# Kernel tuning notes

Measured on AMD Instinct MI355X. Metric: run time of the kernel, lower is better.

Reference implementation:

```python
import jax, jax.numpy as jnp
import numpy as np

B, S, HID, NH, K = 4, 1500, 1024, 16, 64
DH = HID // NH  # 64


def _rel_bias(pos_emb, length):
    # pos_emb: [2K+1, d]; Shaw-style relative position embedding lookup -> [S, S, d]
    kk = (pos_emb.shape[0] - 1) // 2
    idx = jnp.arange(length)
    dist = jnp.clip(idx[None, :] - idx[:, None], -kk, kk) + kk
    return pos_emb[dist]


def setup_inputs() -> dict:
    key = jax.random.key(0)
    ks = jax.random.split(key, 12)
    sq = 1.0 / np.sqrt(HID)
    inp = {
        "query": jax.random.normal(ks[0], (B, S, HID), jnp.float32),
        "key": jax.random.normal(ks[1], (B, S, HID), jnp.float32),
        "value": jax.random.normal(ks[2], (B, S, HID), jnp.float32),
        # per-head QKV projections stacked over heads: [NH, HID, DH]
        "Wq": jax.random.normal(ks[3], (NH, HID, DH), jnp.float32) * sq,
        "bq": jnp.zeros((NH, DH), jnp.float32),
        "Wk": jax.random.normal(ks[4], (NH, HID, DH), jnp.float32) * sq,
        "bk": jnp.zeros((NH, DH), jnp.float32),
        "Wv": jax.random.normal(ks[5], (NH, HID, DH), jnp.float32) * sq,
        "bv": jnp.zeros((NH, DH), jnp.float32),
        # relative position tables [2K+1, DH]
        "pos_k": jax.random.normal(ks[6], (2 * K + 1, DH), jnp.float32) * 0.1,
        "pos_v": jax.random.normal(ks[7], (2 * K + 1, DH), jnp.float32) * 0.1,
        # output projection
        "W_fc": jax.random.normal(ks[8], (HID, HID), jnp.float32) * sq,
        "b_fc": jnp.zeros((HID,), jnp.float32),
    }
    return inp


def reference(query, key, value, Wq, bq, Wk, bk, Wv, bv, pos_k, pos_v, W_fc, b_fc):
    seq = query.shape[1]
    k_bias = _rel_bias(pos_k, seq)  # [S, S, DH]
    v_bias = _rel_bias(pos_v, seq)  # [S, S, DH]

    # batched per-head projections: [B, NH, S, DH]
    q = jnp.einsum('bsh,nhd->bnsd', query, Wq) + bq[None, :, None, :]
    k = jnp.einsum('bsh,nhd->bnsd', key, Wk) + bk[None, :, None, :]
    v = jnp.einsum('bsh,nhd->bnsd', value, Wv) + bv[None, :, None, :]

    attn_1 = jnp.einsum('bnqd,bnkd->bnqk', q, k)
    attn_2 = jnp.einsum('bnqd,qkd->bnqk', q, k_bias)  # Shaw relative key bias
    scores = (attn_1 + attn_2) / jnp.sqrt(jnp.float32(DH))
    w = jax.nn.softmax(scores, axis=-1)  # [B, NH, S, S]

    values_1 = jnp.einsum('bnqk,bnkd->bnqd', w, v)
    values_2 = jnp.einsum('bnqk,qkd->bnqd', w, v_bias)  # Shaw relative value bias
    heads = values_1 + values_2  # [B, NH, S, DH]

    # concat heads in head order -> [B, S, HID]
    hidden = jnp.transpose(heads, (0, 2, 1, 3)).reshape(query.shape[0], seq, -1)
    return hidden @ W_fc + b_fc
```

## Files before the change

kernel.cpp:

```cpp
#include <hip/hip_runtime.h>
#include <stdint.h>

typedef unsigned short u16;
typedef __attribute__((ext_vector_type(8))) short bf16x8;
typedef __attribute__((ext_vector_type(4))) float f32x4;

#define MFMA16(a, b, c) __builtin_amdgcn_mfma_f32_16x16x32_bf16(a, b, c, 0, 0, 0)

__device__ __forceinline__ u16 f2bf(float x) {
  union { float f; uint32_t u; } v; v.f = x;
  uint32_t r = (v.u + 0x7FFFu + ((v.u >> 16) & 1u)) >> 16;
  return (u16)r;
}
__device__ __forceinline__ float bf2f(u16 h) {
  union { uint32_t u; float f; } v; v.u = ((uint32_t)h) << 16; return v.f;
}
__device__ __forceinline__ uint cvt_pk_bf16(float a, float b) {
  uint r;
  asm("v_cvt_pk_bf16_f32 %0, %1, %2" : "=v"(r) : "v"(a), "v"(b));
  return r;
}
__device__ __forceinline__ void gll16(const void* g, void* s) {
  __builtin_amdgcn_global_load_lds((const __attribute__((address_space(1))) unsigned int*)g,
                                   (__attribute__((address_space(3))) unsigned int*)s, 16, 0, 0);
}


__global__ __launch_bounds__(256) void pack_w_kernel(const float* __restrict__ Wq,
                                                     const float* __restrict__ Wk,
                                                     const float* __restrict__ Wv,
                                                     const float* __restrict__ Wfc,
                                                     const float* __restrict__ bq,
                                                     const float* __restrict__ bk,
                                                     const float* __restrict__ bv,
                                                     const float* __restrict__ posk,
                                                     const float* __restrict__ posv,
                                                     u16* __restrict__ Wt,
                                                     u16* __restrict__ Wfct,
                                                     float* __restrict__ biascat,
                                                     u16* __restrict__ poskbf,
                                                     u16* __restrict__ posvT) {
  __shared__ float tile[64][65];
  const int bi = blockIdx.x;
  if (bi == 1024) {
    for (int i = threadIdx.x; i < 1024; i += 256) {
      biascat[i] = bq[i]; biascat[1024 + i] = bk[i]; biascat[2048 + i] = bv[i];
    }
    for (int i = threadIdx.x; i < 144 * 64; i += 256) {
      int r = i >> 6;
      poskbf[i] = (r < 129) ? f2bf(posk[i]) : (u16)0;
    }
    const int d = threadIdx.x & 63, rr = threadIdx.x >> 6;
#pragma unroll
    for (int j = 0; j < 34; ++j) {
      const int r = rr * 34 + j;
      posvT[d * 136 + r] = (r < 129) ? f2bf(posv[(size_t)r * 64 + d]) : (u16)0;
    }
    return;
  }
  const int r = threadIdx.x >> 2, c0 = (threadIdx.x & 3) * 16;
  const float* src;
  u16* outp;
  if (bi < 768) {
    const int z = bi >> 8, rem = bi & 255, n = rem >> 4, h0 = (rem & 15) * 64;
    const float* W = z == 0 ? Wq : (z == 1 ? Wk : Wv);
    src = W + (size_t)n * 65536 + (size_t)(h0 + r) * 64 + c0;
    outp = Wt + (size_t)z * (1024UL * 1024UL) + (size_t)(n * 64 + r) * 1024 + h0 + c0;
  } else {
    const int t = bi - 768;
    const int i0 = (t & 15) * 64, o0 = (t >> 4) * 64;
    src = Wfc + (size_t)(i0 + r) * 1024 + o0 + c0;
    outp = Wfct + (size_t)(o0 + r) * 1024 + i0 + c0;
  }
#pragma unroll
  for (int j = 0; j < 16; j += 4) {
    float4 f = *(const float4*)(src + j);
    tile[r][c0 + j] = f.x; tile[r][c0 + j + 1] = f.y;
    tile[r][c0 + j + 2] = f.z; tile[r][c0 + j + 3] = f.w;
  }
  __syncthreads();
#pragma unroll
  for (int j = 0; j < 16; ++j) outp[j] = f2bf(tile[c0 + j][r]);
}

__global__ __launch_bounds__(256, 4) void gemm_bt_kernel(
    const float* __restrict__ aQ, const float* __restrict__ aK, const float* __restrict__ aV,
    const u16* __restrict__ Ahid,
    const u16* __restrict__ Bbase, long bStride,
    const float* __restrict__ biasBase, long biasStride,
    u16* __restrict__ outBF, u16* __restrict__ VtOut, float* __restrict__ outF, int mode) {
  __shared__ u16 smem[17408];

  const int nwg = 376 * gridDim.z;
  const int cpx = nwg >> 3;
  const int lid = blockIdx.x + (blockIdx.y << 3) + blockIdx.z * 376;
  const int swz = (lid & 7) * cpx + (lid >> 3);
  const int z = swz / 376;
  const int rem = swz - z * 376;
  const int m0 = (rem >> 3) * 128, n0 = (rem & 7) * 128;

  const u16* Bt = Bbase + (size_t)z * bStride;
  const float* bias = biasBase + (size_t)z * biasStride;
  const int tid = threadIdx.x, w = tid >> 6, lane = tid & 63;
  const int quad = lane >> 4, l16 = lane & 15;
  const int wm = w >> 1, wn = w & 1;
  const int srow = w * 16 + (lane >> 2);
  const int scol = (lane & 3) * 8;

  const u16* gB0 = Bt + (size_t)(n0 + srow) * 1024 + scol;
  const u16* gB1 = gB0 + 64UL * 1024;
  const int slab = (w * 16) * 32;

  f32x4 acc[4][4];
  const f32x4 zf = {0.f, 0.f, 0.f, 0.f};
#pragma unroll
  for (int a = 0; a < 4; ++a)
#pragma unroll
    for (int b = 0; b < 4; ++b) acc[a][b] = zf;

  auto gllB = [&](int buf) {
    gll16(gB0, &smem[8192 + buf * 4096 + slab]);
    gll16(gB1, &smem[8192 + buf * 4096 + slab + 64 * 32]);
    gB0 += 32; gB1 += 32;
  };
  auto compute = [&](int buf) {
    bf16x8 af[4], bfr[4];
#pragma unroll
    for (int f = 0; f < 4; ++f) {
      af[f]  = *(const bf16x8*)&smem[buf * 4096 + (wm * 64 + f * 16 + l16) * 32 + quad * 8];
      bfr[f] = *(const bf16x8*)&smem[8192 + buf * 4096 + (wn * 64 + f * 16 + l16) * 32 + quad * 8];
    }
#pragma unroll
    for (int fm = 0; fm < 4; ++fm)
#pragma unroll
      for (int fn = 0; fn < 4; ++fn)
        acc[fm][fn] = MFMA16(af[fm], bfr[fn], acc[fm][fn]);
  };

  if (mode == 0) {
    const float* srcF = z == 0 ? aQ : (z == 1 ? aK : aV);
    int rowA0 = m0 + srow;        if (rowA0 > 5999) rowA0 = 5999;
    int rowA1 = m0 + 64 + srow;   if (rowA1 > 5999) rowA1 = 5999;
    const float* fA0 = srcF + (size_t)rowA0 * 1024 + scol;
    const float* fA1 = srcF + (size_t)rowA1 * 1024 + scol;
    float4 a00, a01, a10, a11;
    auto loadA = [&]() {
      a00 = *(const float4*)fA0; a01 = *(const float4*)(fA0 + 4);
      a10 = *(const float4*)fA1; a11 = *(const float4*)(fA1 + 4);
      fA0 += 32; fA1 += 32;
    };
    const int adst = (w * 16 + (lane >> 2)) * 32 + (lane & 3) * 8;
    auto wrA = [&](int buf) {
      uint4 lo, hi;
      lo.x = cvt_pk_bf16(a00.x, a00.y); lo.y = cvt_pk_bf16(a00.z, a00.w);
      lo.z = cvt_pk_bf16(a01.x, a01.y); lo.w = cvt_pk_bf16(a01.z, a01.w);
      hi.x = cvt_pk_bf16(a10.x, a10.y); hi.y = cvt_pk_bf16(a10.z, a10.w);
      hi.z = cvt_pk_bf16(a11.x, a11.y); hi.w = cvt_pk_bf16(a11.z, a11.w);
      *(uint4*)&smem[buf * 4096 + adst] = lo;
      *(uint4*)&smem[buf * 4096 + adst + 64 * 32] = hi;
    };

    loadA();
    gllB(0);

#pragma unroll 1
    for (int pr = 0; pr < 16; ++pr) {
      asm volatile("s_waitcnt vmcnt(0)" ::: "memory");
      __builtin_amdgcn_sched_barrier(0);
      wrA(0);
      loadA();
      asm volatile("s_waitcnt lgkmcnt(0)" ::: "memory");
      __builtin_amdgcn_sched_barrier(0);
      __builtin_amdgcn_s_barrier();
      __builtin_amdgcn_sched_barrier(0);
      gllB(1);
      compute(0);
      asm volatile("s_waitcnt vmcnt(0)" ::: "memory");
      __builtin_amdgcn_sched_barrier(0);
      wrA(1);
      if (pr < 15) loadA();
      asm volatile("s_waitcnt lgkmcnt(0)" ::: "memory");
      __builtin_amdgcn_sched_barrier(0);
      __builtin_amdgcn_s_barrier();
      __builtin_amdgcn_sched_barrier(0);
      if (pr < 15) gllB(0);
      compute(1);
    }

    if (z < 2) {
      const float scale = (z == 0) ? 0.125f : 1.0f;
      u16* out = outBF + (size_t)z * (4UL * 16 * 1536 * 64);
#pragma unroll
      for (int fm = 0; fm < 4; ++fm) {
#pragma unroll
        for (int i = 0; i < 4; ++i) {
          const int m = m0 + wm * 64 + fm * 16 + quad * 4 + i;
          if (m >= 6000) continue;
          const int bb = m / 1500;
          const int s = m - bb * 1500;
#pragma unroll
          for (int fn = 0; fn < 4; ++fn) {
            const int n = n0 + wn * 64 + fn * 16 + l16;
            const float vv = (acc[fm][fn][i] + bias[n]) * scale;
            const int h = n >> 6, d = n & 63;
            out[((size_t)(bb * 16 + h) * 1536 + s) * 64 + d] = f2bf(vv);
          }
        }
      }
    } else {
      __syncthreads();
      u16* T = smem;
#pragma unroll
      for (int fm = 0; fm < 4; ++fm) {
        const int ml = wm * 64 + fm * 16 + quad * 4;
#pragma unroll
        for (int fn = 0; fn < 4; ++fn) {
          const int nl = wn * 64 + fn * 16 + l16;
          const float b0 = bias[n0 + nl];
          uint2 pk;
          pk.x = cvt_pk_bf16(acc[fm][fn][0] + b0, acc[fm][fn][1] + b0);
          pk.y = cvt_pk_bf16(acc[fm][fn][2] + b0, acc[fm][fn][3] + b0);
          *(uint2*)&T[nl * 136 + ml] = pk;
        }
      }
      __syncthreads();
#pragma unroll 1
      for (int ps = 0; ps < 8; ++ps) {
        const int row = ps * 16 + (tid >> 4);
        const int col = (tid & 15) * 8;
        const int ng = n0 + row;
        const int h = ng >> 6, d = ng & 63;
        const int mg = m0 + col;
        uint4 v = *(const uint4*)&T[row * 136 + col];
        const int bb0 = mg / 1500, bb7 = (mg + 7) / 1500;
        if ((bb0 == bb7) & (mg + 7 < 6000)) {
          u16* dst = VtOut + ((size_t)((bb0 * 16 + h) * 64 + d)) * 1536 + (mg - bb0 * 1500);
          uint2 loh; loh.x = v.x; loh.y = v.y;
          uint2 hih; hih.x = v.z; hih.y = v.w;
          *(uint2*)dst = loh;
          *(uint2*)(dst + 4) = hih;
        } else {
          const u16* tv = (const u16*)&v;
#pragma unroll
          for (int j = 0; j < 8; ++j) {
            const int m = mg + j;
            if (m < 6000) {
              const int bb = m / 1500;
              VtOut[((size_t)((bb * 16 + h) * 64 + d)) * 1536 + (m - bb * 1500)] = tv[j];
            }
          }
        }
      }
    }
  } else {
    const u16* gA0 = Ahid + (size_t)(m0 + srow) * 1024 + scol;
    const u16* gA1 = gA0 + 64UL * 1024;
    auto stage1 = [&](int buf) {
      gll16(gA0, &smem[buf * 4096 + slab]);
      gll16(gA1, &smem[buf * 4096 + slab + 64 * 32]);
      gA0 += 32; gA1 += 32;
      gllB(buf);
    };
    stage1(0);
#define FC_SYNC() do {                                        \
      asm volatile("s_waitcnt vmcnt(0)" ::: "memory");        \
      __builtin_amdgcn_sched_barrier(0);                      \
      __builtin_amdgcn_s_barrier();                           \
      __builtin_amdgcn_sched_barrier(0);                      \
    } while (0)
#pragma unroll 1
    for (int pr = 0; pr < 16; ++pr) {
      FC_SYNC();
      stage1(1);
      compute(0);
      FC_SYNC();
      if (pr < 15) stage1(0);
      compute(1);
    }
#undef FC_SYNC
#pragma unroll
    for (int fm = 0; fm < 4; ++fm) {
#pragma unroll
      for (int i = 0; i < 4; ++i) {
        const int m = m0 + wm * 64 + fm * 16 + quad * 4 + i;
        if (m >= 6000) continue;
#pragma unroll
        for (int fn = 0; fn < 4; ++fn) {
          const int n = n0 + wn * 64 + fn * 16 + l16;
          outF[(size_t)m * 1024 + n] = acc[fm][fn][i] + bias[n];
        }
      }
    }
  }
}

__global__ __launch_bounds__(256, 4) void attn_kernel(const u16* __restrict__ qkv,
                                                      const u16* __restrict__ Vt,
                                                      const u16* __restrict__ poskbf,
                                                      const u16* __restrict__ posvT,
                                                      const float* __restrict__ posv,
                                                      u16* __restrict__ hidden) {
  const size_t ZS = 4UL * 16 * 1536 * 64;
  __shared__ u16 qb_s[64 * 136];
  __shared__ u16 kbuf[2][2048];
  __shared__ u16 vbuf[2][2048];

  const int tid = threadIdx.x;
  const int w = tid >> 6, lane = tid & 63, quad = lane >> 4, l16 = lane & 15;
  const int bi = blockIdx.x;
  const int bh = bi & 63;
  const int q0 = (bi >> 6) * 64, qw0 = q0 + w * 16;
  const int b = bh >> 4;
  const size_t sb = (size_t)bh * (1536UL * 64UL);
  const u16* Qp = qkv + sb;
  const u16* Kp = qkv + ZS + sb;
  const u16* Vtb = Vt + (size_t)bh * (64UL * 1536UL);
  u16* qb_row = qb_s + (w * 16 + l16) * 136;

  const int r8 = lane >> 3, c8 = lane & 7;
  const int vr = lane >> 2, vc = lane & 3;
  const int kprow = ((( (w * 8 + r8) & 15) >> 2) * 8) + (((w * 8 + r8) >> 4) * 4) + ((w * 8 + r8) & 3);
  const u16* kSrc = Kp + (size_t)kprow * 64 + ((c8 ^ r8) * 8);
  const u16* vSrc = Vtb + (size_t)(w * 16 + vr) * 1536 + ((vc ^ ((vr >> 1) & 3)) * 8);
  u16* const kDst = &kbuf[0][0] + w * 512;
  u16* const vDst = &vbuf[0][0] + w * 512;

  gll16(kSrc, kDst);
  gll16(vSrc, vDst);

  const u16* qptr = Qp + (size_t)(qw0 + l16) * 64 + quad * 8;
  const bf16x8 qB0 = *(const bf16x8*)qptr;
  const bf16x8 qB1 = *(const bf16x8*)(qptr + 32);

  const f32x4 zf = {0.f, 0.f, 0.f, 0.f};
#pragma unroll
  for (int nf = 0; nf < 9; ++nf) {
    const u16* bp = poskbf + (size_t)(nf * 16 + l16) * 64 + quad * 8;
    bf16x8 b0 = *(const bf16x8*)bp;
    bf16x8 b1 = *(const bf16x8*)(bp + 32);
    f32x4 c = zf;
    c = MFMA16(qB0, b0, c);
    c = MFMA16(qB1, b1, c);
    const int col = nf * 16 + l16;
    if (col < 136) {
#pragma unroll
      for (int i = 0; i < 4; ++i)
        qb_s[(w * 16 + quad * 4 + i) * 136 + col] = f2bf(c[i]);
    }
  }
  __syncthreads();

  const float L2E = 1.44269504f;
  const float M8 = -8.0f * L2E;
  const float eLow  = __builtin_fmaf(bf2f(qb_row[0]), L2E, M8);
  const float eHigh = __builtin_fmaf(bf2f(qb_row[128]), L2E, M8);

  f32x4 accf[4];
#pragma unroll
  for (int dc = 0; dc < 4; ++dc) accf[dc] = zf;
  float sSimple = 0.f, sLowSave = 0.f, sDall = 0.f, sD0 = 0.f, sD128 = 0.f;

  const int itLowEnd = (qw0 >= 95) ? (((qw0 - 95) >> 5) + 1) : 0;
  const int itHigh0 = (qw0 + 110) >> 5;
  const int dEnd = itHigh0 < 46 ? itHigh0 : 46;

  const int kswz = (quad ^ (l16 & 7)) * 8;
  const int kswz4 = ((quad + 4) ^ (l16 & 7)) * 8;
  const int vpos = (quad ^ ((l16 >> 1) & 3)) * 8;

  const u16* kS = kSrc + 2048;
  const u16* vS = vSrc + 32;

  auto body = [&](int it, const u16* kb, const u16* vbse, bool doStage, int stageOff) {
    if (doStage) {
      gll16(kS, kDst + stageOff);
      gll16(vS, vDst + stageOff);
      kS += 2048; vS += 32;
    }

    if (it == itLowEnd) sLowSave = sSimple;
    const int phase = (it < itLowEnd) ? 0 : ((it >= 46) ? 1 : ((it < dEnd) ? 1 : 2));

    bf16x8 ka00 = *(const bf16x8*)(kb + l16 * 64 + kswz);
    bf16x8 ka01 = *(const bf16x8*)(kb + l16 * 64 + kswz4);
    bf16x8 ka10 = *(const bf16x8*)(kb + (16 + l16) * 64 + kswz);
    bf16x8 ka11 = *(const bf16x8*)(kb + (16 + l16) * 64 + kswz4);
    bf16x8 vb0 = *(const bf16x8*)(vbse + l16 * 32 + vpos);
    bf16x8 vb1 = *(const bf16x8*)(vbse + (16 + l16) * 32 + vpos);
    bf16x8 vb2 = *(const bf16x8*)(vbse + (32 + l16) * 32 + vpos);
    bf16x8 vb3 = *(const bf16x8*)(vbse + (48 + l16) * 32 + vpos);

    float qb[2][4];
    if (phase == 1) {
      const int base = it * 32 + 64 - qw0 - l16 + quad * 8;
#pragma unroll
      for (int cg = 0; cg < 2; ++cg) {
#pragma unroll
        for (int i = 0; i < 4; ++i) {
          int delta = base + cg * 4 + i;
          delta = delta < 0 ? 0 : (delta > 128 ? 128 : delta);
          qb[cg][i] = bf2f(qb_row[delta]);
        }
      }
    }

    f32x4 cc[2];
    cc[0] = zf; cc[1] = zf;
    cc[0] = MFMA16(ka00, qB0, cc[0]);
    cc[0] = MFMA16(ka01, qB1, cc[0]);
    cc[1] = MFMA16(ka10, qB0, cc[1]);
    cc[1] = MFMA16(ka11, qB1, cc[1]);

    float pvv[2][4];
    if (phase != 1) {
      const float eB = (phase == 0) ? eLow : eHigh;
#pragma unroll
      for (int cg = 0; cg < 2; ++cg) {
#pragma unroll
        for (int i = 0; i < 4; ++i) {
          float p = __builtin_amdgcn_exp2f(__builtin_fmaf(cc[cg][i], L2E, eB));
          sSimple += p; pvv[cg][i] = p;
        }
      }
    } else {
      const int kc0 = it * 32;
#pragma unroll
      for (int cg = 0; cg < 2; ++cg) {
        const int krow0 = kc0 + quad * 8 + cg * 4;
        const int dbase = krow0 + 64 - qw0 - l16;
#pragma unroll
        for (int i = 0; i < 4; ++i) {
          int delta = dbase + i;
          delta = delta < 0 ? 0 : (delta > 128 ? 128 : delta);
          const float t = cc[cg][i] + qb[cg][i];
          float p = __builtin_amdgcn_exp2f(__builtin_fmaf(t, L2E, M8));
          if (krow0 + i >= 1500) p = 0.f;
          sDall += p;
          sD0   += (delta == 0)   ? p : 0.f;
          sD128 += (delta == 128) ? p : 0.f;
          pvv[cg][i] = p;
        }
        const uint pk01 = cvt_pk_bf16(pvv[cg][0], pvv[cg][1]);
        const uint pk23 = cvt_pk_bf16(pvv[cg][2], pvv[cg][3]);
        const u16 hb[4] = {(u16)pk01, (u16)(pk01 >> 16), (u16)pk23, (u16)(pk23 >> 16)};
#pragma unroll
        for (int i = 0; i < 4; ++i) {
          int delta = dbase + i;
          delta = delta < 0 ? 0 : (delta > 128 ? 128 : delta);
          if ((delta != 0) & (delta != 128)) qb_row[delta] = hb[i];
        }
      }
    }

    union { uint u[4]; bf16x8 v; } pa;
    pa.u[0] = cvt_pk_bf16(pvv[0][0], pvv[0][1]);
    pa.u[1] = cvt_pk_bf16(pvv[0][2], pvv[0][3]);
    pa.u[2] = cvt_pk_bf16(pvv[1][0], pvv[1][1]);
    pa.u[3] = cvt_pk_bf16(pvv[1][2], pvv[1][3]);

    accf[0] = MFMA16(pa.v, vb0, accf[0]);
    accf[1] = MFMA16(pa.v, vb1, accf[1]);
    accf[2] = MFMA16(pa.v, vb2, accf[2]);
    accf[3] = MFMA16(pa.v, vb3, accf[3]);

    __syncthreads();
  };

#pragma unroll 1
  for (int pr = 0; pr < 23; ++pr) {
    const int it0 = pr * 2;
    body(it0,     &kbuf[0][0], &vbuf[0][0], true, 2048);
    body(it0 + 1, &kbuf[1][0], &vbuf[1][0], true, 0);
  }
  body(46, &kbuf[0][0], &vbuf[0][0], false, 0);

  const float sLow = sLowSave;
  const float sHigh = sSimple - sLowSave;
  float lpart = sSimple + sDall;
  float clow = sLow + sD0;
  float chigh = sHigh + sD128;
#pragma unroll
  for (int m = 16; m <= 32; m <<= 1) {
    lpart += __shfl_xor(lpart, m);
    clow  += __shfl_xor(clow, m);
    chigh += __shfl_xor(chigh, m);
  }
  const float linv = 1.0f / lpart;

  {
    const int qg_row = qw0 + l16;
    if (quad == 0) qb_row[0] = 0;
    const int lim = 64 - qg_row;
    for (int d = 1 + quad; d < lim; d += 4) qb_row[d] = 0;
    const int dlo = 1564 - qg_row;
    for (int d = dlo + quad; d <= 127; d += 4) qb_row[d] = 0;
  }

  f32x4 o2[4];
#pragma unroll
  for (int dc = 0; dc < 4; ++dc) o2[dc] = zf;
#pragma unroll
  for (int kk = 0; kk < 4; ++kk) {
    bf16x8 pa2 = *(const bf16x8*)(qb_row + kk * 32 + quad * 8);
#pragma unroll
    for (int dc = 0; dc < 4; ++dc) {
      bf16x8 vb2r = *(const bf16x8*)(posvT + (size_t)(dc * 16 + l16) * 136 + kk * 32 + quad * 8);
      o2[dc] = MFMA16(pa2, vb2r, o2[dc]);
    }
  }

  float li[4], cl[4], ch[4];
#pragma unroll
  for (int i = 0; i < 4; ++i) {
    const int srcl = quad * 4 + i;
    li[i] = __shfl(linv, srcl);
    cl[i] = __shfl(clow, srcl);
    ch[i] = __shfl(chigh, srcl);
  }

#pragma unroll
  for (int dc = 0; dc < 4; ++dc) {
    const int d = dc * 16 + l16;
    const float pv0 = posv[d], pv1 = posv[128 * 64 + d];
#pragma unroll
    for (int i = 0; i < 4; ++i) {
      const int qg = qw0 + quad * 4 + i;
      if (qg < 1500) {
        const float val = (accf[dc][i] + o2[dc][i] + cl[i] * pv0 + ch[i] * pv1) * li[i];
        hidden[((size_t)(b * 1500 + qg)) * 1024 + (bh & 15) * 64 + d] = f2bf(val);
      }
    }
  }
}

extern "C" void kernel_launch(void* const* d_in, const int* in_sizes, int n_in,
                              void* d_out, int out_size, void* d_ws, size_t ws_size,
                              hipStream_t stream) {
  const float* query = (const float*)d_in[0];
  const float* key   = (const float*)d_in[1];
  const float* value = (const float*)d_in[2];
  const float* Wq = (const float*)d_in[3];
  const float* bq = (const float*)d_in[4];
  const float* Wk = (const float*)d_in[5];
  const float* bk = (const float*)d_in[6];
  const float* Wv = (const float*)d_in[7];
  const float* bv = (const float*)d_in[8];
  const float* posk = (const float*)d_in[9];
  const float* posv = (const float*)d_in[10];
  const float* Wfc = (const float*)d_in[11];
  const float* bfc = (const float*)d_in[12];
  float* out = (float*)d_out;

  char* p = (char*)d_ws;
  u16* X = (u16*)p;        p += 3UL * 6016 * 1024 * 2;
  u16* Wt = (u16*)p;       p += 3UL * 1024 * 1024 * 2;
  u16* Wfct = (u16*)p;     p += 1024UL * 1024 * 2;
  u16* poskbf = (u16*)p;   p += 144UL * 64 * 2;
  u16* posvT = (u16*)p;    p += 64UL * 136 * 2;
  float* biascat = (float*)p; p += 3UL * 1024 * 4;
  u16* qkv = (u16*)p;      p += 3UL * 4 * 16 * 1536 * 64 * 2;
  u16* hidden = X;
  u16* Vt = X + 6291456;

  pack_w_kernel<<<dim3(1025), 256, 0, stream>>>(Wq, Wk, Wv, Wfc, bq, bk, bv, posk, posv,
                                                Wt, Wfct, biascat, poskbf, posvT);

  gemm_bt_kernel<<<dim3(8, 47, 3), 256, 0, stream>>>(
      query, key, value, nullptr, Wt, 1024L * 1024, biascat, 1024L, qkv, Vt, nullptr, 0);

  attn_kernel<<<dim3(1536), 256, 0, stream>>>(qkv, Vt, poskbf, posvT, posv, hidden);

  gemm_bt_kernel<<<dim3(8, 47, 1), 256, 0, stream>>>(
      nullptr, nullptr, nullptr, hidden, Wfct, 0L, bfc, 0L, nullptr, nullptr, out, 1);
}
```

Before: 346.2 us.

## Split output projection into dedicated kernel with four-stage async load pipeline

Moves the final FC GEMM out of the shared mode-switched GEMM kernel into its own kernel. The new kernel uses four LDS buffers and issues global-to-LDS loads three k-steps ahead, waiting with partial vmcnt counts instead of draining all loads each step. The intent is to hide memory latency in the output projection and drop the mode branch and unused parameters from the QKV GEMM. Launch bounds drop to 2 blocks per CU because of the larger shared memory footprint, which may reduce occupancy.

```diff
diff --git a/kernel.cpp b/kernel.cpp
--- a/kernel.cpp
+++ b/kernel.cpp
@@ -85,10 +85,9 @@
 
 __global__ __launch_bounds__(256, 4) void gemm_bt_kernel(
     const float* __restrict__ aQ, const float* __restrict__ aK, const float* __restrict__ aV,
-    const u16* __restrict__ Ahid,
     const u16* __restrict__ Bbase, long bStride,
     const float* __restrict__ biasBase, long biasStride,
-    u16* __restrict__ outBF, u16* __restrict__ VtOut, float* __restrict__ outF, int mode) {
+    u16* __restrict__ outBF, u16* __restrict__ VtOut) {
   __shared__ u16 smem[17408];
 
   const int nwg = 376 * gridDim.z;
@@ -137,158 +136,207 @@
         acc[fm][fn] = MFMA16(af[fm], bfr[fn], acc[fm][fn]);
   };
 
-  if (mode == 0) {
-    const float* srcF = z == 0 ? aQ : (z == 1 ? aK : aV);
-    int rowA0 = m0 + srow;        if (rowA0 > 5999) rowA0 = 5999;
-    int rowA1 = m0 + 64 + srow;   if (rowA1 > 5999) rowA1 = 5999;
-    const float* fA0 = srcF + (size_t)rowA0 * 1024 + scol;
-    const float* fA1 = srcF + (size_t)rowA1 * 1024 + scol;
-    float4 a00, a01, a10, a11;
-    auto loadA = [&]() {
-      a00 = *(const float4*)fA0; a01 = *(const float4*)(fA0 + 4);
-      a10 = *(const float4*)fA1; a11 = *(const float4*)(fA1 + 4);
-      fA0 += 32; fA1 += 32;
-    };
-    const int adst = (w * 16 + (lane >> 2)) * 32 + (lane & 3) * 8;
-    auto wrA = [&](int buf) {
-      uint4 lo, hi;
-      lo.x = cvt_pk_bf16(a00.x, a00.y); lo.y = cvt_pk_bf16(a00.z, a00.w);
-      lo.z = cvt_pk_bf16(a01.x, a01.y); lo.w = cvt_pk_bf16(a01.z, a01.w);
-      hi.x = cvt_pk_bf16(a10.x, a10.y); hi.y = cvt_pk_bf16(a10.z, a10.w);
-      hi.z = cvt_pk_bf16(a11.x, a11.y); hi.w = cvt_pk_bf16(a11.z, a11.w);
-      *(uint4*)&smem[buf * 4096 + adst] = lo;
-      *(uint4*)&smem[buf * 4096 + adst + 64 * 32] = hi;
-    };
-
+  const float* srcF = z == 0 ? aQ : (z == 1 ? aK : aV);
+  int rowA0 = m0 + srow;        if (rowA0 > 5999) rowA0 = 5999;
+  int rowA1 = m0 + 64 + srow;   if (rowA1 > 5999) rowA1 = 5999;
+  const float* fA0 = srcF + (size_t)rowA0 * 1024 + scol;
+  const float* fA1 = srcF + (size_t)rowA1 * 1024 + scol;
+  float4 a00, a01, a10, a11;
+  auto loadA = [&]() {
+    a00 = *(const float4*)fA0; a01 = *(const float4*)(fA0 + 4);
+    a10 = *(const float4*)fA1; a11 = *(const float4*)(fA1 + 4);
+    fA0 += 32; fA1 += 32;
+  };
+  const int adst = (w * 16 + (lane >> 2)) * 32 + (lane & 3) * 8;
+  auto wrA = [&](int buf) {
+    uint4 lo, hi;
+    lo.x = cvt_pk_bf16(a00.x, a00.y); lo.y = cvt_pk_bf16(a00.z, a00.w);
+    lo.z = cvt_pk_bf16(a01.x, a01.y); lo.w = cvt_pk_bf16(a01.z, a01.w);
+    hi.x = cvt_pk_bf16(a10.x, a10.y); hi.y = cvt_pk_bf16(a10.z, a10.w);
+    hi.z = cvt_pk_bf16(a11.x, a11.y); hi.w = cvt_pk_bf16(a11.z, a11.w);
+    *(uint4*)&smem[buf * 4096 + adst] = lo;
+    *(uint4*)&smem[buf * 4096 + adst + 64 * 32] = hi;
+  };
+
+  loadA();
+  gllB(0);
+
+#pragma unroll 1
+  for (int pr = 0; pr < 16; ++pr) {
+    asm volatile("s_waitcnt vmcnt(0)" ::: "memory");
+    __builtin_amdgcn_sched_barrier(0);
+    wrA(0);
     loadA();
-    gllB(0);
-
-#pragma unroll 1
-    for (int pr = 0; pr < 16; ++pr) {
-      asm volatile("s_waitcnt vmcnt(0)" ::: "memory");
-      __builtin_amdgcn_sched_barrier(0);
-      wrA(0);
-      loadA();
-      asm volatile("s_waitcnt lgkmcnt(0)" ::: "memory");
-      __builtin_amdgcn_sched_barrier(0);
-      __builtin_amdgcn_s_barrier();
-      __builtin_amdgcn_sched_barrier(0);
-      gllB(1);
-      compute(0);
-      asm volatile("s_waitcnt vmcnt(0)" ::: "memory");
-      __builtin_amdgcn_sched_barrier(0);
-      wrA(1);
-      if (pr < 15) loadA();
-      asm volatile("s_waitcnt lgkmcnt(0)" ::: "memory");
-      __builtin_amdgcn_sched_barrier(0);
-      __builtin_amdgcn_s_barrier();
-      __builtin_amdgcn_sched_barrier(0);
-      if (pr < 15) gllB(0);
-      compute(1);
-    }
-
-    if (z < 2) {
-      const float scale = (z == 0) ? 0.125f : 1.0f;
-      u16* out = outBF + (size_t)z * (4UL * 16 * 1536 * 64);
-#pragma unroll
-      for (int fm = 0; fm < 4; ++fm) {
-#pragma unroll
-        for (int i = 0; i < 4; ++i) {
-          const int m = m0 + wm * 64 + fm * 16 + quad * 4 + i;
-          if (m >= 6000) continue;
-          const int bb = m / 1500;
-          const int s = m - bb * 1500;
-#pragma unroll
-          for (int fn = 0; fn < 4; ++fn) {
-            const int n = n0 + wn * 64 + fn * 16 + l16;
-            const float vv = (acc[fm][fn][i] + bias[n]) * scale;
-            const int h = n >> 6, d = n & 63;
-            out[((size_t)(bb * 16 + h) * 1536 + s) * 64 + d] = f2bf(vv);
-          }
-        }
-      }
-    } else {
-      __syncthreads();
-      u16* T = smem;
-#pragma unroll
-      for (int fm = 0; fm < 4; ++fm) {
-        const int ml = wm * 64 + fm * 16 + quad * 4;
-#pragma unroll
-        for (int fn = 0; fn < 4; ++fn) {
-          const int nl = wn * 64 + fn * 16 + l16;
-          const float b0 = bias[n0 + nl];
-          uint2 pk;
-          pk.x = cvt_pk_bf16(acc[fm][fn][0] + b0, acc[fm][fn][1] + b0);
-          pk.y = cvt_pk_bf16(acc[fm][fn][2] + b0, acc[fm][fn][3] + b0);
-          *(uint2*)&T[nl * 136 + ml] = pk;
-        }
-      }
-      __syncthreads();
-#pragma unroll 1
-      for (int ps = 0; ps < 8; ++ps) {
-        const int row = ps * 16 + (tid >> 4);
-        const int col = (tid & 15) * 8;
-        const int ng = n0 + row;
-        const int h = ng >> 6, d = ng & 63;
-        const int mg = m0 + col;
-        uint4 v = *(const uint4*)&T[row * 136 + col];
-        const int bb0 = mg / 1500, bb7 = (mg + 7) / 1500;
-        if ((bb0 == bb7) & (mg + 7 < 6000)) {
-          u16* dst = VtOut + ((size_t)((bb0 * 16 + h) * 64 + d)) * 1536 + (mg - bb0 * 1500);
-          uint2 loh; loh.x = v.x; loh.y = v.y;
-          uint2 hih; hih.x = v.z; hih.y = v.w;
-          *(uint2*)dst = loh;
-          *(uint2*)(dst + 4) = hih;
-        } else {
-          const u16* tv = (const u16*)&v;
-#pragma unroll
-          for (int j = 0; j < 8; ++j) {
-            const int m = mg + j;
-            if (m < 6000) {
-              const int bb = m / 1500;
-              VtOut[((size_t)((bb * 16 + h) * 64 + d)) * 1536 + (m - bb * 1500)] = tv[j];
-            }
-          }
-        }
-      }
-    }
-  } else {
-    const u16* gA0 = Ahid + (size_t)(m0 + srow) * 1024 + scol;
-    const u16* gA1 = gA0 + 64UL * 1024;
-    auto stage1 = [&](int buf) {
-      gll16(gA0, &smem[buf * 4096 + slab]);
-      gll16(gA1, &smem[buf * 4096 + slab + 64 * 32]);
-      gA0 += 32; gA1 += 32;
-      gllB(buf);
-    };
-    stage1(0);
-#define FC_SYNC() do {                                        \
-      asm volatile("s_waitcnt vmcnt(0)" ::: "memory");        \
-      __builtin_amdgcn_sched_barrier(0);                      \
-      __builtin_amdgcn_s_barrier();                           \
-      __builtin_amdgcn_sched_barrier(0);                      \
-    } while (0)
-#pragma unroll 1
-    for (int pr = 0; pr < 16; ++pr) {
-      FC_SYNC();
-      stage1(1);
-      compute(0);
-      FC_SYNC();
-      if (pr < 15) stage1(0);
-      compute(1);
-    }
-#undef FC_SYNC
+    asm volatile("s_waitcnt lgkmcnt(0)" ::: "memory");
+    __builtin_amdgcn_sched_barrier(0);
+    __builtin_amdgcn_s_barrier();
+    __builtin_amdgcn_sched_barrier(0);
+    gllB(1);
+    compute(0);
+    asm volatile("s_waitcnt vmcnt(0)" ::: "memory");
+    __builtin_amdgcn_sched_barrier(0);
+    wrA(1);
+    if (pr < 15) loadA();
+    asm volatile("s_waitcnt lgkmcnt(0)" ::: "memory");
+    __builtin_amdgcn_sched_barrier(0);
+    __builtin_amdgcn_s_barrier();
+    __builtin_amdgcn_sched_barrier(0);
+    if (pr < 15) gllB(0);
+    compute(1);
+  }
+
+  if (z < 2) {
+    const float scale = (z == 0) ? 0.125f : 1.0f;
+    u16* out = outBF + (size_t)z * (4UL * 16 * 1536 * 64);
 #pragma unroll
     for (int fm = 0; fm < 4; ++fm) {
 #pragma unroll
       for (int i = 0; i < 4; ++i) {
         const int m = m0 + wm * 64 + fm * 16 + quad * 4 + i;
         if (m >= 6000) continue;
+        const int bb = m / 1500;
+        const int s = m - bb * 1500;
 #pragma unroll
         for (int fn = 0; fn < 4; ++fn) {
           const int n = n0 + wn * 64 + fn * 16 + l16;
-          outF[(size_t)m * 1024 + n] = acc[fm][fn][i] + bias[n];
+          const float vv = (acc[fm][fn][i] + bias[n]) * scale;
+          const int h = n >> 6, d = n & 63;
+          out[((size_t)(bb * 16 + h) * 1536 + s) * 64 + d] = f2bf(vv);
         }
+      }
+    }
+  } else {
+    __syncthreads();
+    u16* T = smem;
+#pragma unroll
+    for (int fm = 0; fm < 4; ++fm) {
+      const int ml = wm * 64 + fm * 16 + quad * 4;
+#pragma unroll
+      for (int fn = 0; fn < 4; ++fn) {
+        const int nl = wn * 64 + fn * 16 + l16;
+        const float b0 = bias[n0 + nl];
+        uint2 pk;
+        pk.x = cvt_pk_bf16(acc[fm][fn][0] + b0, acc[fm][fn][1] + b0);
+        pk.y = cvt_pk_bf16(acc[fm][fn][2] + b0, acc[fm][fn][3] + b0);
+        *(uint2*)&T[nl * 136 + ml] = pk;
+      }
+    }
+    __syncthreads();
+#pragma unroll 1
+    for (int ps = 0; ps < 8; ++ps) {
+      const int row = ps * 16 + (tid >> 4);
+      const int col = (tid & 15) * 8;
+      const int ng = n0 + row;
+      const int h = ng >> 6, d = ng & 63;
+      const int mg = m0 + col;
+      uint4 v = *(const uint4*)&T[row * 136 + col];
+      const int bb0 = mg / 1500, bb7 = (mg + 7) / 1500;
+      if ((bb0 == bb7) & (mg + 7 < 6000)) {
+        u16* dst = VtOut + ((size_t)((bb0 * 16 + h) * 64 + d)) * 1536 + (mg - bb0 * 1500);
+        uint2 loh; loh.x = v.x; loh.y = v.y;
+        uint2 hih; hih.x = v.z; hih.y = v.w;
+        *(uint2*)dst = loh;
+        *(uint2*)(dst + 4) = hih;
+      } else {
+        const u16* tv = (const u16*)&v;
+#pragma unroll
+        for (int j = 0; j < 8; ++j) {
+          const int m = mg + j;
+          if (m < 6000) {
+            const int bb = m / 1500;
+            VtOut[((size_t)((bb * 16 + h) * 64 + d)) * 1536 + (m - bb * 1500)] = tv[j];
+          }
+        }
+      }
+    }
+  }
+}
+
+__global__ __launch_bounds__(256, 2) void fc_kernel(const u16* __restrict__ Ahid,
+                                                    const u16* __restrict__ Bt,
+                                                    const float* __restrict__ bias,
+                                                    float* __restrict__ outF) {
+  __shared__ u16 As[4][4096];
+  __shared__ u16 Bs[4][4096];
+
+  const int lid = blockIdx.x + (blockIdx.y << 3);
+  const int swz = (lid & 7) * 47 + (lid >> 3);
+  const int m0 = (swz >> 3) * 128, n0 = (swz & 7) * 128;
+
+  const int tid = threadIdx.x, w = tid >> 6, lane = tid & 63;
+  const int quad = lane >> 4, l16 = lane & 15;
+  const int wm = w >> 1, wn = w & 1;
+  const int srow = w * 16 + (lane >> 2);
+  const int scol = (lane & 3) * 8;
+
+  const u16* gA0 = Ahid + (size_t)(m0 + srow) * 1024 + scol;
+  const u16* gA1 = gA0 + 64UL * 1024;
+  const u16* gB0 = Bt + (size_t)(n0 + srow) * 1024 + scol;
+  const u16* gB1 = gB0 + 64UL * 1024;
+  const int slab = w * 512;
+
+  f32x4 acc[4][4];
+  const f32x4 zf = {0.f, 0.f, 0.f, 0.f};
+#pragma unroll
+  for (int a = 0; a < 4; ++a)
+#pragma unroll
+    for (int b = 0; b < 4; ++b) acc[a][b] = zf;
+
+  auto stage = [&](int buf) {
+    gll16(gA0, &As[buf][slab]);
+    gll16(gA1, &As[buf][slab + 2048]);
+    gll16(gB0, &Bs[buf][slab]);
+    gll16(gB1, &Bs[buf][slab + 2048]);
+    gA0 += 32; gA1 += 32; gB0 += 32; gB1 += 32;
+  };
+  auto compute = [&](int buf) {
+    bf16x8 af[4], bfr[4];
+#pragma unroll
+    for (int f = 0; f < 4; ++f) {
+      af[f]  = *(const bf16x8*)&As[buf][(wm * 64 + f * 16 + l16) * 32 + quad * 8];
+      bfr[f] = *(const bf16x8*)&Bs[buf][(wn * 64 + f * 16 + l16) * 32 + quad * 8];
+    }
+#pragma unroll
+    for (int fm = 0; fm < 4; ++fm)
+#pragma unroll
+      for (int fn = 0; fn < 4; ++fn)
+        acc[fm][fn] = MFMA16(af[fm], bfr[fn], acc[fm][fn]);
+  };
+
+  stage(0); stage(1); stage(2);
+
+#define FC_BODY(BUF, N, DOSTAGE, SBUF) do {                   \
+    asm volatile("s_waitcnt vmcnt(" #N ")" ::: "memory");     \
+    __builtin_amdgcn_sched_barrier(0);                        \
+    __builtin_amdgcn_s_barrier();                             \
+    __builtin_amdgcn_sched_barrier(0);                        \
+    if (DOSTAGE) stage(SBUF);                                 \
+    compute(BUF);                                             \
+  } while (0)
+
+#pragma unroll 1
+  for (int pr = 0; pr < 7; ++pr) {
+    FC_BODY(0, 8, true, 3);
+    FC_BODY(1, 8, true, 0);
+    FC_BODY(2, 8, true, 1);
+    FC_BODY(3, 8, true, 2);
+  }
+  FC_BODY(0, 8, true, 3);
+  FC_BODY(1, 8, false, 0);
+  FC_BODY(2, 4, false, 0);
+  FC_BODY(3, 0, false, 0);
+#undef FC_BODY
+
+#pragma unroll
+  for (int fm = 0; fm < 4; ++fm) {
+#pragma unroll
+    for (int i = 0; i < 4; ++i) {
+      const int m = m0 + wm * 64 + fm * 16 + quad * 4 + i;
+      if (m >= 6000) continue;
+#pragma unroll
+      for (int fn = 0; fn < 4; ++fn) {
+        const int n = n0 + wn * 64 + fn * 16 + l16;
+        outF[(size_t)m * 1024 + n] = acc[fm][fn][i] + bias[n];
       }
     }
   }
@@ -566,10 +614,9 @@
                                                 Wt, Wfct, biascat, poskbf, posvT);
 
   gemm_bt_kernel<<<dim3(8, 47, 3), 256, 0, stream>>>(
-      query, key, value, nullptr, Wt, 1024L * 1024, biascat, 1024L, qkv, Vt, nullptr, 0);
+      query, key, value, Wt, 1024L * 1024, biascat, 1024L, qkv, Vt);
 
   attn_kernel<<<dim3(1536), 256, 0, stream>>>(qkv, Vt, poskbf, posvT, posv, hidden);
 
-  gemm_bt_kernel<<<dim3(8, 47, 1), 256, 0, stream>>>(
-      nullptr, nullptr, nullptr, hidden, Wfct, 0L, bfc, 0L, nullptr, nullptr, out, 1);
-}
+  fc_kernel<<<dim3(8, 47), 256, 0, stream>>>(hidden, Wfct, bfc, out);
+}
```

After: 332.3 us. -4.0%, faster.
